# Kernel optimization log

Hardware: AMD Instinct MI355X
Metric: run time of the kernel (lower is better)

The kernel has to match this reference:

```python
import jax, jax.numpy as jnp
import numpy as np

B, S, D, H, DH = 2, 4096, 768, 12, 64
L = 2                      # encoder layers (reduced-depth longformer-base)
HW = 256                   # one-sided sliding window (attention_window = 512)
C = 2 * HW                 # query chunk size
NC = S // C                # number of chunks
KW = C + 2 * HW            # key-window length per chunk
V = 50265
SEP_ID, NSEP = 2, 32       # </s> token id; SEPs per block (fixed by construction)
G = NSEP + 1               # global tokens: <s> at pos 0 + all SEPs
NCLS = 5
EPS = 1e-5
NEG = -1e9


def layer_norm(x, gb):
    m = jnp.mean(x, -1, keepdims=True)
    v = jnp.var(x, -1, keepdims=True)
    return (x - m) * jax.lax.rsqrt(v + EPS) * gb[0] + gb[1]


def split_heads(x):  # [B,S,D] -> [B,H,S,DH]
    return x.reshape(B, S, H, DH).transpose(0, 2, 1, 3)


def window_gather(x):  # [B,H,S,DH] -> [B,H,NC,KW,DH] overlapping key windows
    xp = jnp.pad(x, ((0, 0), (0, 0), (HW, HW), (0, 0)))
    idx = (jnp.arange(NC) * C)[:, None] + jnp.arange(KW)[None, :]
    return xp[:, :, idx, :]


def longformer_attn(x, amask, gpos, wqkv, bqkv, wqkv_g, bqkv_g, wo, bo):
    q = split_heads(x @ wqkv[0] + bqkv[0]) / np.float32(np.sqrt(DH))
    k = split_heads(x @ wqkv[1] + bqkv[1])
    v = split_heads(x @ wqkv[2] + bqkv[2])

    # ----- local sliding-window scores (banded, chunked) -----
    kw = window_gather(k)
    vw = window_gather(v)
    qc = q.reshape(B, H, NC, C, DH)
    s_loc = jnp.einsum('bhncd,bhnkd->bhnck', qc, kw)  # [B,H,NC,C,KW]

    rel = jnp.arange(KW)[None, :] - jnp.arange(C)[:, None]          # [C,KW]
    band_ok = (rel >= 0) & (rel <= 2 * HW)
    key_pos = (jnp.arange(NC) * C)[:, None] + jnp.arange(KW)[None, :] - HW
    in_b = (key_pos >= 0) & (key_pos < S)                            # [NC,KW]
    amp = jnp.pad(amask, ((0, 0), (HW, HW)))
    idx = (jnp.arange(NC) * C)[:, None] + jnp.arange(KW)[None, :]
    am_w = amp[:, idx] > 0                                           # [B,NC,KW]
    mask = band_ok[None, None, None] & in_b[None, None, :, None, :] & am_w[:, None, :, None, :]
    s_loc = jnp.where(mask, s_loc, NEG).reshape(B, H, S, KW)

    # ----- scores of every query against the G global keys -----
    gidx = gpos[:, None, :, None]                                    # [B,1,G,1]
    kg = jnp.take_along_axis(k, gidx, axis=2)                        # [B,H,G,DH]
    vg = jnp.take_along_axis(v, gidx, axis=2)
    s_glob = jnp.einsum('bhsd,bhgd->bhsg', q, kg)                    # [B,H,S,G]

    probs = jax.nn.softmax(jnp.concatenate([s_glob, s_loc], -1), -1)
    pg, pl = probs[..., :G], probs[..., G:]
    ctx = jnp.einsum('bhsg,bhgd->bhsd', pg, vg)
    ctx = ctx + jnp.einsum('bhnck,bhnkd->bhncd', pl.reshape(B, H, NC, C, KW), vw).reshape(B, H, S, DH)

    # ----- global tokens attend to everything (separate projections) -----
    qg = split_heads(x @ wqkv_g[0] + bqkv_g[0]) / np.float32(np.sqrt(DH))
    kgf = split_heads(x @ wqkv_g[1] + bqkv_g[1])
    vgf = split_heads(x @ wqkv_g[2] + bqkv_g[2])
    qg = jnp.take_along_axis(qg, gidx, axis=2)                       # [B,H,G,DH]
    s_g = jnp.einsum('bhgd,bhsd->bhgs', qg, kgf)                     # [B,H,G,S]
    s_g = jnp.where(amask[:, None, None, :] > 0, s_g, NEG)
    og = jnp.einsum('bhgs,bhsd->bhgd', jax.nn.softmax(s_g, -1), vgf)

    ctx_m = ctx.transpose(0, 2, 1, 3).reshape(B, S, D)
    og_m = og.transpose(0, 2, 1, 3).reshape(B, G, D)
    ctx_m = ctx_m.at[jnp.arange(B)[:, None], gpos].set(og_m)         # replace global rows
    return ctx_m @ wo + bo


def setup_inputs() -> dict:
    key = jax.random.key(0)
    ks = jax.random.split(key, 12)
    ids = jax.random.randint(ks[0], (B, S), 5, V, dtype=jnp.int32)
    sep_positions = (jnp.arange(NSEP) + 1) * (S // NSEP) - 1         # SEP every 128 toks
    ids = ids.at[:, sep_positions].set(SEP_ID).at[:, 0].set(0)       # <s> at pos 0
    att = jnp.ones((B, S), jnp.int32)

    def nrm(k, shp):
        return jax.random.normal(k, shp, jnp.float32) * 0.02

    ln = jnp.stack([jnp.ones(D, jnp.float32), jnp.zeros(D, jnp.float32)])
    return dict(
        input_ids=ids, attention_mask=att,
        word_emb=nrm(ks[1], (V, D)), pos_emb=nrm(ks[2], (S + 2, D)),
        type_emb=nrm(ks[3], (D,)), emb_ln=ln,
        Wqkv=nrm(ks[4], (L, 3, D, D)), bqkv=jnp.zeros((L, 3, D), jnp.float32),
        Wqkv_g=nrm(ks[5], (L, 3, D, D)), bqkv_g=jnp.zeros((L, 3, D), jnp.float32),
        Wo=nrm(ks[6], (L, D, D)), bo=jnp.zeros((L, D), jnp.float32),
        ln1=jnp.broadcast_to(ln, (L, 2, D)),
        Wff1=nrm(ks[7], (L, D, 4 * D)), bff1=jnp.zeros((L, 4 * D), jnp.float32),
        Wff2=nrm(ks[8], (L, 4 * D, D)), bff2=jnp.zeros((L, D), jnp.float32),
        ln2=jnp.broadcast_to(ln, (L, 2, D)),
        cls_W=nrm(ks[9], (NCLS, D)), cls_b=jnp.zeros((NCLS,), jnp.float32),
    )


def reference(input_ids, attention_mask, word_emb, pos_emb, type_emb, emb_ln,
              Wqkv, bqkv, Wqkv_g, bqkv_g, Wo, bo, ln1, Wff1, bff1, Wff2, bff2,
              ln2, cls_W, cls_b):
    # global attention mask: pos 0 + every SEP (fixed count by construction)
    sep_pos = jnp.sort(jnp.where(input_ids == SEP_ID, jnp.arange(S)[None, :], S), -1)[:, :NSEP]
    sep_pos = sep_pos.astype(jnp.int32)
    gpos = jnp.concatenate([jnp.zeros((B, 1), jnp.int32), sep_pos], 1)  # [B,G]

    x = word_emb[input_ids] + pos_emb[jnp.arange(S) + 2][None] + type_emb
    x = layer_norm(x, emb_ln)
    for l in range(L):
        a = longformer_attn(x, attention_mask, gpos, Wqkv[l], bqkv[l],
                            Wqkv_g[l], bqkv_g[l], Wo[l], bo[l])
        x = layer_norm(x + a, ln1[l])
        f = jax.nn.gelu(x @ Wff1[l] + bff1[l], approximate=False) @ Wff2[l] + bff2[l]
        x = layer_norm(x + f, ln2[l])

    # gather SEP embeddings (row-major over batch then sentence) -> classifier
    h = jnp.take_along_axis(x, sep_pos[:, :, None], axis=1).reshape(B * NSEP, D)
    return h @ cls_W.T + cls_b
```

## Files before the change

### kernel.cpp

```cpp
#include <hip/hip_runtime.h>


#define Bb 2
#define Ss 4096
#define Dd 768
#define Hh 12
#define Gg 33
#define NSEPn 32
#define Ll 2
#define SPAD 4640
#define PADL 256
#define NCLSn 5
#define NCH 16
#define PARTF 1056
#define PSTR 72

typedef unsigned short u16;
typedef __attribute__((ext_vector_type(8))) short bv8;
typedef __attribute__((ext_vector_type(4))) short sv4;
typedef __attribute__((ext_vector_type(4))) float f32x4;

__device__ __forceinline__ float bf2f(u16 u) {
  unsigned v = ((unsigned)u) << 16;
  return __builtin_bit_cast(float, v);
}
__device__ __forceinline__ u16 f2bf(float f) {
  unsigned u = __builtin_bit_cast(unsigned, f);
  u += 0x7fffu + ((u >> 16) & 1u);
  return (u16)(u >> 16);
}
__device__ __forceinline__ void glds16(const void* g, void* l) {
  __builtin_amdgcn_global_load_lds(
      (const __attribute__((address_space(1))) void*)g,
      (__attribute__((address_space(3))) void*)l, 16, 0, 0);
}

__global__ void sep_find_kernel(const int* __restrict__ ids, int* __restrict__ cnt,
                                int* __restrict__ list) {
  int i = blockIdx.x * 256 + threadIdx.x;
  if (i >= Bb * Ss) return;
  int b = i >> 12;
  if (ids[i] == 2) {
    int idx = atomicAdd(&cnt[b], 1);
    if (idx < 64) list[b * 64 + idx] = i & (Ss - 1);
  }
}

__global__ void sep_sort_kernel(const int* __restrict__ cnt, const int* __restrict__ list,
                                int* __restrict__ gpos) {
  int b = blockIdx.x;
  int t = threadIdx.x;
  int n = cnt[b]; if (n > 64) n = 64;
  if (t < Gg) gpos[b * Gg + t] = (t == 0) ? 0 : (Ss - 1);
  __syncthreads();
  if (t < n) {
    int v = list[b * 64 + t];
    int rank = 0;
    for (int j = 0; j < n; ++j) rank += (list[b * 64 + j] < v) ? 1 : 0;
    if (rank < NSEPn) gpos[b * Gg + 1 + rank] = v;
  }
}

__global__ __launch_bounds__(256)
void wconv_kernel(const float* __restrict__ src0, u16* __restrict__ dst0,
                  int K, int N, int grp, int sstr, long unit, long WLs) {
  __shared__ float t[32][33];
  int z = blockIdx.z;
  const float* src = src0 + (size_t)((z / grp) * sstr + (z % grp)) * K * N;
  u16* dst = dst0 + (size_t)(z / grp) * WLs + (size_t)(z % grp) * unit;
  int n0 = blockIdx.x * 32, k0 = blockIdx.y * 32;
  int tx = threadIdx.x & 31, ty = threadIdx.x >> 5;
  #pragma unroll
  for (int i = 0; i < 4; ++i)
    t[ty + i * 8][tx] = src[(size_t)(k0 + ty + i * 8) * N + n0 + tx];
  __syncthreads();
  #pragma unroll
  for (int i = 0; i < 4; ++i)
    dst[(size_t)(n0 + ty + i * 8) * K + k0 + tx] = f2bf(t[tx][ty + i * 8]);
}

__global__ __launch_bounds__(256)
void embed_ln_kernel(const int* __restrict__ ids, const float* __restrict__ we,
                     const float* __restrict__ pe, const float* __restrict__ te,
                     const float* __restrict__ lnp, float* __restrict__ x,
                     u16* __restrict__ xb) {
  int row = blockIdx.x;
  int s = row & (Ss - 1);
  int id = ids[row];
  int tid = threadIdx.x;
  float v[3]; float sm = 0.f, s2 = 0.f;
  #pragma unroll
  for (int i = 0; i < 3; ++i) {
    int c = tid + i * 256;
    float t = we[(size_t)id * Dd + c] + pe[(size_t)(s + 2) * Dd + c] + te[c];
    v[i] = t; sm += t; s2 += t * t;
  }
  __shared__ float r1[256], r2[256];
  r1[tid] = sm; r2[tid] = s2; __syncthreads();
  for (int o = 128; o; o >>= 1) {
    if (tid < o) { r1[tid] += r1[tid + o]; r2[tid] += r2[tid + o]; }
    __syncthreads();
  }
  float mean = r1[0] * (1.f / 768.f);
  float var  = r2[0] * (1.f / 768.f) - mean * mean;
  float rs = rsqrtf(var + 1e-5f);
  #pragma unroll
  for (int i = 0; i < 3; ++i) {
    int c = tid + i * 256;
    float o = (v[i] - mean) * rs * lnp[c] + lnp[Dd + c];
    x[(size_t)row * Dd + c] = o;
    xb[(size_t)row * Dd + c] = f2bf(o);
  }
}

__global__ __launch_bounds__(256)
void add_ln3_kernel(const float* __restrict__ xin, const float* __restrict__ y0,
                    const float* __restrict__ y1, const float* __restrict__ lnp,
                    float* __restrict__ xout, u16* __restrict__ xbout) {
  int row = blockIdx.x;
  int tid = threadIdx.x;
  float v[3]; float sm = 0.f, s2 = 0.f;
  #pragma unroll
  for (int i = 0; i < 3; ++i) {
    int c = tid + i * 256;
    size_t idx = (size_t)row * Dd + c;
    float t = xin[idx] + y0[idx] + y1[idx];
    v[i] = t; sm += t; s2 += t * t;
  }
  __shared__ float r1[256], r2[256];
  r1[tid] = sm; r2[tid] = s2; __syncthreads();
  for (int o = 128; o; o >>= 1) {
    if (tid < o) { r1[tid] += r1[tid + o]; r2[tid] += r2[tid + o]; }
    __syncthreads();
  }
  float mean = r1[0] * (1.f / 768.f);
  float var  = r2[0] * (1.f / 768.f) - mean * mean;
  float rs = rsqrtf(var + 1e-5f);
  #pragma unroll
  for (int i = 0; i < 3; ++i) {
    int c = tid + i * 256;
    float o = (v[i] - mean) * rs * lnp[c] + lnp[Dd + c];
    xout[(size_t)row * Dd + c] = o;
    xbout[(size_t)row * Dd + c] = f2bf(o);
  }
}

template <int MODE, bool XSWZ>
__global__ __launch_bounds__(256)
void gemm2_kernel(const u16* __restrict__ A, const u16* __restrict__ Bt,
                  const float* __restrict__ bias, float* __restrict__ outf,
                  float* __restrict__ outf2,
                  u16* __restrict__ o0, u16* __restrict__ o1, u16* __restrict__ o2,
                  u16* __restrict__ o3, u16* __restrict__ o4,
                  int N, int Ks, int Kl, float scale) {
  __shared__ u16 la[2][128 * 32], lb[2][128 * 32];
  int tid = threadIdx.x;
  int wave = tid >> 6, lane = tid & 63;
  int wr = wave >> 1, wc = wave & 1;
  int lg = lane >> 4, lc = lane & 15;
  int bx = blockIdx.x, by = blockIdx.y;
  if (XSWZ) {
    int gx = gridDim.x;
    int nlin = bx + gx * by;
    int NB = gx * gridDim.y;
    nlin = (nlin & 7) * (NB >> 3) + (nlin >> 3);
    bx = nlin % gx;
    by = nlin / gx;
  }
  int row0 = by * 128, col0 = bx * 128;
  int koff = blockIdx.z * Kl;

  int sgr = (lane & 3) ^ ((lane >> 3) & 3);
  const u16* Ag = A + (size_t)(row0 + wave * 32 + (lane >> 2)) * Ks + sgr * 8 + koff;
  const u16* Bg = Bt + (size_t)(col0 + wave * 32 + (lane >> 2)) * Ks + sgr * 8 + koff;
  int wofs = wave * 1024;
  int gph = (lg ^ ((lc >> 1) & 3)) * 8;

  f32x4 acc[4][4];
  #pragma unroll
  for (int m = 0; m < 4; ++m)
    #pragma unroll
    for (int n = 0; n < 4; ++n) acc[m][n] = (f32x4){0.f, 0.f, 0.f, 0.f};

  glds16(Ag, la[0] + wofs);
  glds16(Ag + (size_t)16 * Ks, la[0] + wofs + 512);
  glds16(Bg, lb[0] + wofs);
  glds16(Bg + (size_t)16 * Ks, lb[0] + wofs + 512);
  __syncthreads();

  int nk = Kl >> 5;
  for (int t = 0; t < nk; ++t) {
    int cur = t & 1;
    if (t + 1 < nk) {
      int k1 = (t + 1) << 5;
      glds16(Ag + k1, la[cur ^ 1] + wofs);
      glds16(Ag + (size_t)16 * Ks + k1, la[cur ^ 1] + wofs + 512);
      glds16(Bg + k1, lb[cur ^ 1] + wofs);
      glds16(Bg + (size_t)16 * Ks + k1, lb[cur ^ 1] + wofs + 512);
    }
    bv8 af[4], bf_[4];
    #pragma unroll
    for (int m = 0; m < 4; ++m)
      af[m] = *reinterpret_cast<const bv8*>(la[cur] + (wr * 64 + m * 16 + lc) * 32 + gph);
    #pragma unroll
    for (int n = 0; n < 4; ++n)
      bf_[n] = *reinterpret_cast<const bv8*>(lb[cur] + (wc * 64 + n * 16 + lc) * 32 + gph);
    __builtin_amdgcn_s_setprio(1);
    #pragma unroll
    for (int m = 0; m < 4; ++m)
      #pragma unroll
      for (int n = 0; n < 4; ++n)
        acc[m][n] = __builtin_amdgcn_mfma_f32_16x16x32_bf16(af[m], bf_[n], acc[m][n], 0, 0, 0);
    __builtin_amdgcn_s_setprio(0);
    __syncthreads();
  }

  #pragma unroll
  for (int m = 0; m < 4; ++m) {
    int grow0 = row0 + wr * 64 + m * 16 + lg * 4;
    #pragma unroll
    for (int n = 0; n < 4; ++n) {
      int gcol = col0 + wc * 64 + n * 16 + lc;
      float bvl = bias[gcol];
      if (MODE == 0) {
        float* od = blockIdx.z ? outf2 : outf;
        float badd = blockIdx.z ? 0.f : bvl;
        #pragma unroll
        for (int r = 0; r < 4; ++r)
          od[(size_t)(grow0 + r) * N + gcol] = acc[m][n][r] + badd;
      } else if (MODE == 1) {
        #pragma unroll
        for (int r = 0; r < 4; ++r) {
          float v = acc[m][n][r] + bvl;
          v = 0.5f * v * (1.0f + erff(v * 0.70710678118654752f));
          o0[(size_t)(grow0 + r) * N + gcol] = f2bf(v);
        }
      } else if (MODE == 4) {
        #pragma unroll
        for (int r = 0; r < 4; ++r)
          o0[(size_t)(grow0 + r) * N + gcol] = f2bf((acc[m][n][r] + bvl) * scale);
      } else if (MODE == 2) {
        int sec = (col0 >> 7) / 6;
        int colr = gcol - sec * 768;
        int hh = colr >> 6, d = colr & 63;
        int bb = grow0 >> 12, s = grow0 & (Ss - 1);
        size_t bhh = (size_t)(bb * Hh + hh);
        if (sec == 0) {
          #pragma unroll
          for (int r = 0; r < 4; ++r)
            o0[(bhh * Ss + s + r) * 64 + d] = f2bf((acc[m][n][r] + bvl) * scale);
        } else if (sec == 1) {
          #pragma unroll
          for (int r = 0; r < 4; ++r)
            o1[(bhh * SPAD + PADL + s + r) * 64 + d] = f2bf(acc[m][n][r] + bvl);
        } else if (sec == 2) {
          sv4 pk;
          #pragma unroll
          for (int r = 0; r < 4; ++r) pk[r] = (short)f2bf(acc[m][n][r] + bvl);
          *reinterpret_cast<sv4*>(o2 + (bhh * 64 + d) * SPAD + PADL + s) = pk;
        } else if (sec == 3) {
          #pragma unroll
          for (int r = 0; r < 4; ++r)
            o3[(bhh * Ss + s + r) * 64 + d] = f2bf(acc[m][n][r] + bvl);
        } else {
          sv4 pk;
          #pragma unroll
          for (int r = 0; r < 4; ++r) pk[r] = (short)f2bf(acc[m][n][r] + bvl);
          *reinterpret_cast<sv4*>(o4 + (bhh * 64 + d) * Ss + s) = pk;
        }
      }
    }
  }
}

__global__ __launch_bounds__(256)
void gather_glob_kernel(const u16* __restrict__ kpk, const u16* __restrict__ vtpk,
                        const int* __restrict__ gpos, u16* __restrict__ kg,
                        u16* __restrict__ vgt) {
  int bh = blockIdx.x;
  int b = bh / Hh;
  int tid = threadIdx.x;
  for (int idx = tid; idx < 64 * 64; idx += 256) {
    int g = idx >> 6, d = idx & 63;
    u16 kv = 0, vv = 0;
    if (g < Gg) {
      int p = gpos[b * Gg + g];
      kv = kpk[((size_t)bh * SPAD + PADL + p) * 64 + d];
      vv = vtpk[((size_t)bh * 64 + d) * SPAD + PADL + p];
    }
    kg[(size_t)bh * 4096 + idx] = kv;
    vgt[((size_t)bh * 64 + d) * 64 + g] = vv;
  }
}

__global__ __launch_bounds__(256)
void gather_xg_kernel(const u16* __restrict__ xb, const int* __restrict__ gpos,
                      u16* __restrict__ xg) {
  int rg = blockIdx.x;
  int b = rg / Gg;
  int p = gpos[rg];
  int tid = threadIdx.x;
  for (int c = tid; c < Dd; c += 256)
    xg[(size_t)rg * Dd + c] = xb[((size_t)b * Ss + p) * Dd + c];
}

#define LOCAL_NB (Bb * Hh * (Ss / 64))
__global__ __launch_bounds__(256)
void attn_local_kernel(const u16* __restrict__ qpk, const u16* __restrict__ kpk,
                       const u16* __restrict__ vtpk, const u16* __restrict__ kg,
                       const u16* __restrict__ vgt, const int* __restrict__ amask,
                       u16* __restrict__ ctx) {
  __shared__ u16 Plds[4][16 * PSTR];
  int bid = blockIdx.x;
  int swz = (bid & 7) * (LOCAL_NB / 8) + (bid >> 3);
  int qb = swz & 63;
  int bh = swz >> 6;
  int b = bh / Hh;
  int h = bh - b * Hh;
  int wv = threadIdx.x >> 6;
  int q0 = qb * 64 + wv * 16;
  int lane = threadIdx.x & 63;
  int lg = lane >> 4, lc = lane & 15;
  int lg4 = lg * 4;
  int q = q0 + lc;

  const u16* qbase = qpk + (((size_t)bh) * Ss + q0) * 64;
  bv8 aq0 = *reinterpret_cast<const bv8*>(qbase + (size_t)lc * 64 + lg * 8);
  bv8 aq1 = *reinterpret_cast<const bv8*>(qbase + (size_t)lc * 64 + 32 + lg * 8);

  f32x4 o[4];
  #pragma unroll
  for (int i = 0; i < 4; ++i) o[i] = (f32x4){0.f, 0.f, 0.f, 0.f};
  float mrun = -1e30f, lrun = 0.f;

  const u16* kgb = kg + ((size_t)bh) * 64 * 64;
  const u16* vgb = vgt + ((size_t)bh) * 64 * 64;
  const u16* kb = kpk + ((size_t)bh) * SPAD * 64;
  const u16* vb = vtpk + ((size_t)bh) * 64 * SPAD;
  const int* amb = amask + b * Ss;
  u16* P = &Plds[wv][0];

  bv8 kc[8];
  #pragma unroll
  for (int j = 0; j < 4; ++j) {
    const u16* kr = kgb + (size_t)(j * 16 + lc) * 64;
    kc[2 * j]     = *reinterpret_cast<const bv8*>(kr + lg * 8);
    kc[2 * j + 1] = *reinterpret_cast<const bv8*>(kr + 32 + lg * 8);
  }
  int amvN;
  { int ni = min(max(q0 - 256 + lane, 0), Ss - 1); amvN = amb[ni]; }

  for (int step = 0; step < 10; ++step) {
    bool isg = (step == 0);
    int ks = isg ? 0 : (q0 - 256 + (step - 1) * 64);
    int amvC = amvN;
    if (step < 9) { int ni = min(max(q0 - 256 + step * 64 + lane, 0), Ss - 1); amvN = amb[ni]; }

    bv8 vf[8];
    #pragma unroll
    for (int j2 = 0; j2 < 2; ++j2)
      #pragma unroll
      for (int nt = 0; nt < 4; ++nt) {
        const u16* vr = isg ? (vgb + (size_t)(nt * 16 + lc) * 64 + j2 * 32)
                            : (vb + (size_t)(nt * 16 + lc) * SPAD + PADL + ks + j2 * 32);
        vf[j2 * 4 + nt] = *reinterpret_cast<const bv8*>(vr + lg * 8);
      }
    unsigned long long kmask;
    if (isg) {
      kmask = (1ull << Gg) - 1;
    } else {
      int kidx = ks + lane;
      kmask = __ballot((kidx >= 0) && (kidx < Ss) && (amvC > 0));
    }
    f32x4 sc[4];
    __builtin_amdgcn_s_setprio(1);
    #pragma unroll
    for (int j = 0; j < 4; ++j) {
      f32x4 z = (f32x4){0.f, 0.f, 0.f, 0.f};
      sc[j] = __builtin_amdgcn_mfma_f32_16x16x32_bf16(kc[2 * j], aq0, z, 0, 0, 0);
      sc[j] = __builtin_amdgcn_mfma_f32_16x16x32_bf16(kc[2 * j + 1], aq1, sc[j], 0, 0, 0);
    }
    __builtin_amdgcn_s_setprio(0);
    if (step < 9) {
      int ksn = q0 - 256 + step * 64;
      #pragma unroll
      for (int j = 0; j < 4; ++j) {
        const u16* kr = kb + (size_t)(PADL + ksn + j * 16 + lc) * 64;
        kc[2 * j]     = *reinterpret_cast<const bv8*>(kr + lg * 8);
        kc[2 * j + 1] = *reinterpret_cast<const bv8*>(kr + 32 + lg * 8);
      }
    }
    float mloc = -1e30f;
    bool fast = (!isg) && (step >= 2) && (step <= 8) && (kmask == ~0ull);
    if (fast) {
      #pragma unroll
      for (int j = 0; j < 4; ++j)
        #pragma unroll
        for (int r = 0; r < 4; ++r) mloc = fmaxf(mloc, sc[j][r]);
    } else {
      #pragma unroll
      for (int j = 0; j < 4; ++j)
        #pragma unroll
        for (int r = 0; r < 4; ++r) {
          int kk = ks + j * 16 + lg4 + r;
          bool ok = (kmask >> (j * 16 + lg4 + r)) & 1;
          if (!isg) ok = ok && ((unsigned)(kk - q + 256) <= 512u);
          sc[j][r] = ok ? sc[j][r] : -1e9f;
          mloc = fmaxf(mloc, sc[j][r]);
        }
    }
    mloc = fmaxf(mloc, __shfl_xor(mloc, 16));
    mloc = fmaxf(mloc, __shfl_xor(mloc, 32));
    if (__any(mloc > mrun)) {
      float nm = fmaxf(mrun, mloc);
      float scal = __expf(mrun - nm);
      mrun = nm;
      lrun *= scal;
      #pragma unroll
      for (int r = 0; r < 4; ++r) {
        float sr = __shfl(scal, lg4 + r);
        #pragma unroll
        for (int nt = 0; nt < 4; ++nt) o[nt][r] *= sr;
      }
    }
    float psum = 0.f;
    #pragma unroll
    for (int j = 0; j < 4; ++j) {
      sv4 pk;
      #pragma unroll
      for (int r = 0; r < 4; ++r) {
        float p = __expf(sc[j][r] - mrun);
        psum += p;
        pk[r] = (short)f2bf(p);
      }
      *reinterpret_cast<sv4*>(P + lc * PSTR + j * 16 + lg4) = pk;
    }
    psum += __shfl_xor(psum, 16);
    psum += __shfl_xor(psum, 32);
    lrun += psum;
    __builtin_amdgcn_s_setprio(1);
    #pragma unroll
    for (int j2 = 0; j2 < 2; ++j2) {
      bv8 ap = *reinterpret_cast<const bv8*>(P + lc * PSTR + j2 * 32 + lg * 8);
      #pragma unroll
      for (int nt = 0; nt < 4; ++nt)
        o[nt] = __builtin_amdgcn_mfma_f32_16x16x32_bf16(ap, vf[j2 * 4 + nt], o[nt], 0, 0, 0);
    }
    __builtin_amdgcn_s_setprio(0);
  }
  float inv = 1.0f / lrun;
  #pragma unroll
  for (int r = 0; r < 4; ++r) {
    float invr = __shfl(inv, lg4 + r);
    size_t rowoff = ((size_t)b * Ss + q0 + lg4 + r) * Dd + h * 64;
    #pragma unroll
    for (int nt = 0; nt < 4; ++nt)
      ctx[rowoff + nt * 16 + lc] = f2bf(o[nt][r] * invr);
  }
}

__global__ __launch_bounds__(192)
void attn_globalq_kernel(const u16* __restrict__ qgb, const u16* __restrict__ kgf,
                         const u16* __restrict__ vgt, const int* __restrict__ amask,
                         float* __restrict__ part) {
  __shared__ u16 Plds[3][16 * 32];
  int blk = blockIdx.x;
  int ch = blk & (NCH - 1);
  int bh = blk / NCH;
  int b = bh / Hh, h = bh - b * Hh;
  int wv = threadIdx.x >> 6;
  int lane = threadIdx.x & 63;
  int lg = lane >> 4, lc = lane & 15;

  int qrow = wv * 16 + lc;
  bv8 aq0 = (bv8)0, aq1 = (bv8)0;
  if (qrow < Gg) {
    const u16* qr = qgb + (size_t)(b * Gg + qrow) * Dd + h * 64;
    aq0 = *reinterpret_cast<const bv8*>(qr + lg * 8);
    aq1 = *reinterpret_cast<const bv8*>(qr + 32 + lg * 8);
  }

  f32x4 o[4];
  float mrun[4], lrun[4];
  #pragma unroll
  for (int i = 0; i < 4; ++i) { o[i] = (f32x4){0.f,0.f,0.f,0.f}; mrun[i] = -1e30f; lrun[i] = 0.f; }

  const u16* kb = kgf + ((size_t)bh) * Ss * 64;
  const u16* vb = vgt + ((size_t)bh) * 64 * Ss;
  const int* amb = amask + b * Ss;
  int ks0 = ch * (Ss / NCH);

  for (int st = 0; st < (Ss / NCH) / 32; ++st) {
    int ks = ks0 + st * 32;
    f32x4 sc0, sc1;
    {
      const u16* kr0 = kb + (size_t)(ks + lc) * 64;
      const u16* kr1 = kr0 + 16 * 64;
      bv8 b00 = *reinterpret_cast<const bv8*>(kr0 + lg * 8);
      bv8 b01 = *reinterpret_cast<const bv8*>(kr0 + 32 + lg * 8);
      bv8 b10 = *reinterpret_cast<const bv8*>(kr1 + lg * 8);
      bv8 b11 = *reinterpret_cast<const bv8*>(kr1 + 32 + lg * 8);
      f32x4 z = (f32x4){0.f,0.f,0.f,0.f};
      sc0 = __builtin_amdgcn_mfma_f32_16x16x32_bf16(aq0, b00, z, 0, 0, 0);
      sc0 = __builtin_amdgcn_mfma_f32_16x16x32_bf16(aq1, b01, sc0, 0, 0, 0);
      sc1 = __builtin_amdgcn_mfma_f32_16x16x32_bf16(aq0, b10, z, 0, 0, 0);
      sc1 = __builtin_amdgcn_mfma_f32_16x16x32_bf16(aq1, b11, sc1, 0, 0, 0);
    }
    bool v0 = amb[ks + lc] > 0;
    bool v1 = amb[ks + 16 + lc] > 0;
    #pragma unroll
    for (int r = 0; r < 4; ++r) {
      float s0 = v0 ? sc0[r] : -1e9f;
      float s1 = v1 ? sc1[r] : -1e9f;
      float rm = fmaxf(s0, s1);
      #pragma unroll
      for (int off = 1; off < 16; off <<= 1) rm = fmaxf(rm, __shfl_xor(rm, off));
      float nm = fmaxf(mrun[r], rm);
      float scal = __expf(mrun[r] - nm);
      float p0 = __expf(s0 - nm);
      float p1 = __expf(s1 - nm);
      float ps = p0 + p1;
      #pragma unroll
      for (int off = 1; off < 16; off <<= 1) ps += __shfl_xor(ps, off);
      lrun[r] = lrun[r] * scal + ps;
      mrun[r] = nm;
      #pragma unroll
      for (int nt = 0; nt < 4; ++nt) o[nt][r] *= scal;
      int prow = lg * 4 + r;
      Plds[wv][prow * 32 + lc] = f2bf(p0);
      Plds[wv][prow * 32 + 16 + lc] = f2bf(p1);
    }
    bv8 ap = *reinterpret_cast<const bv8*>(&Plds[wv][lc * 32 + lg * 8]);
    #pragma unroll
    for (int nt = 0; nt < 4; ++nt) {
      const u16* vr = vb + (size_t)(nt * 16 + lc) * Ss + ks;
      bv8 bvv = *reinterpret_cast<const bv8*>(vr + lg * 8);
      o[nt] = __builtin_amdgcn_mfma_f32_16x16x32_bf16(ap, bvv, o[nt], 0, 0, 0);
    }
  }

  float* pb = part + ((size_t)(bh * 3 + wv) * NCH + ch) * PARTF;
  #pragma unroll
  for (int r = 0; r < 4; ++r) {
    int row = lg * 4 + r;
    #pragma unroll
    for (int nt = 0; nt < 4; ++nt)
      pb[row * 64 + nt * 16 + lc] = o[nt][r];
    if (lc == 0) {
      pb[1024 + row] = mrun[r];
      pb[1040 + row] = lrun[r];
    }
  }
}

__global__ __launch_bounds__(256)
void attn_gmerge_kernel(const float* __restrict__ part, const int* __restrict__ gpos,
                        u16* __restrict__ ctx) {
  __shared__ float wgt[Gg][NCH];
  __shared__ float sinvl[Gg];
  int bh = blockIdx.x;
  int b = bh / Hh, h = bh - b * Hh;
  int tid = threadIdx.x;
  if (tid < Gg) {
    int qt = tid >> 4, rr = tid & 15;
    const float* pb = part + ((size_t)(bh * 3 + qt) * NCH) * PARTF;
    float mx = -1e30f;
    for (int c = 0; c < NCH; ++c) mx = fmaxf(mx, pb[c * PARTF + 1024 + rr]);
    float l = 0.f;
    for (int c = 0; c < NCH; ++c) {
      float w = __expf(pb[c * PARTF + 1024 + rr] - mx);
      wgt[tid][c] = w;
      l += w * pb[c * PARTF + 1040 + rr];
    }
    sinvl[tid] = 1.0f / l;
  }
  __syncthreads();
  for (int e = tid; e < Gg * 64; e += 256) {
    int row = e >> 6, d = e & 63;
    int qt = row >> 4, rr = row & 15;
    const float* pb = part + ((size_t)(bh * 3 + qt) * NCH) * PARTF + rr * 64 + d;
    float acc = 0.f;
    #pragma unroll
    for (int c = 0; c < NCH; ++c) acc += wgt[row][c] * pb[c * PARTF];
    int pos = gpos[b * Gg + row];
    ctx[((size_t)b * Ss + pos) * Dd + h * 64 + d] = f2bf(acc * sinvl[row]);
  }
}

__global__ __launch_bounds__(64)
void cls_kernel(const float* __restrict__ x, const float* __restrict__ W,
                const float* __restrict__ bias, const int* __restrict__ gpos,
                float* __restrict__ out) {
  int r = blockIdx.x;
  int b = r >> 5, i = r & 31;
  int pos = gpos[b * Gg + 1 + i];
  int lane = threadIdx.x;
  const float* xr = x + ((size_t)b * Ss + pos) * Dd;
  float acc[NCLSn] = {0.f, 0.f, 0.f, 0.f, 0.f};
  for (int k = lane; k < Dd; k += 64) {
    float xv = xr[k];
    #pragma unroll
    for (int c = 0; c < NCLSn; ++c) acc[c] += xv * W[c * Dd + k];
  }
  #pragma unroll
  for (int c = 0; c < NCLSn; ++c) {
    #pragma unroll
    for (int off = 1; off < 64; off <<= 1) acc[c] += __shfl_xor(acc[c], off);
  }
  if (lane == 0) {
    #pragma unroll
    for (int c = 0; c < NCLSn; ++c) out[r * NCLSn + c] = acc[c] + bias[c];
  }
}

extern "C" void kernel_launch(void* const* d_in, const int* in_sizes, int n_in,
                              void* d_out, int out_size, void* d_ws, size_t ws_size,
                              hipStream_t stream) {
  const int* ids     = (const int*)d_in[0];
  const int* amask   = (const int*)d_in[1];
  const float* we    = (const float*)d_in[2];
  const float* pe    = (const float*)d_in[3];
  const float* te    = (const float*)d_in[4];
  const float* embln = (const float*)d_in[5];
  const float* Wqkv  = (const float*)d_in[6];
  const float* bqkv  = (const float*)d_in[7];
  const float* Wqkvg = (const float*)d_in[8];
  const float* bqkvg = (const float*)d_in[9];
  const float* Wo    = (const float*)d_in[10];
  const float* bo    = (const float*)d_in[11];
  const float* ln1   = (const float*)d_in[12];
  const float* Wff1  = (const float*)d_in[13];
  const float* bff1  = (const float*)d_in[14];
  const float* Wff2  = (const float*)d_in[15];
  const float* bff2  = (const float*)d_in[16];
  const float* ln2   = (const float*)d_in[17];
  const float* clsW  = (const float*)d_in[18];
  const float* clsb  = (const float*)d_in[19];
  float* out = (float*)d_out;

  char* ws = (char*)d_ws;
  size_t off = 0;
  auto alloc = [&](size_t bytes) { size_t o = off; off += (bytes + 255) & ~(size_t)255; return o; };

  const size_t DD = (size_t)Dd * Dd;
  const size_t DF = (size_t)Dd * 4 * Dd;
  const size_t WL = 7 * DD + 2 * DF;

  size_t o_cnt  = alloc(Bb * 4);
  size_t o_list = alloc(Bb * 64 * 4);
  size_t o_gpos = alloc(Bb * Gg * 4);
  size_t o_bias = alloc((size_t)Ll * 3840 * 4);
  size_t o_w    = alloc(WL * Ll * 2);
  size_t o_x    = alloc((size_t)Bb * Ss * Dd * 4);
  size_t o_xb   = alloc((size_t)Bb * Ss * Dd * 2);
  size_t o_kgf  = alloc((size_t)Bb * Hh * Ss * 64 * 2);
  size_t o_vgf  = alloc((size_t)Bb * Hh * Ss * 64 * 2);
  size_t o_accB = o_kgf;
  size_t o_qpk  = alloc((size_t)Bb * Hh * Ss * 64 * 2);
  size_t o_kpk  = alloc((size_t)Bb * Hh * SPAD * 64 * 2);
  size_t o_vtpk = alloc((size_t)Bb * Hh * 64 * SPAD * 2);
  size_t o_kg   = alloc((size_t)Bb * Hh * 64 * 64 * 2);
  size_t o_vgt  = alloc((size_t)Bb * Hh * 64 * 64 * 2);
  size_t o_xg   = alloc((size_t)128 * Dd * 2);
  size_t o_qg   = alloc((size_t)128 * Dd * 2);
  size_t o_part = alloc((size_t)Bb * Hh * 3 * NCH * PARTF * 4);
  size_t o_f1b  = o_qpk;
  {
    size_t f1b_bytes = (size_t)Bb * Ss * 4 * Dd * 2;
    if (off - o_qpk < f1b_bytes) off = o_qpk + ((f1b_bytes + 255) & ~(size_t)255);
  }
  size_t o_ctx = alloc((size_t)Bb * Ss * Dd * 2);
  size_t o_acc = alloc((size_t)Bb * Ss * Dd * 4);
  if (ws_size < off) return;

  u16* Wb = (u16*)(ws + o_w);
  int* gposp = (int*)(ws + o_gpos);
  float* accA = (float*)(ws + o_acc);
  float* accB = (float*)(ws + o_accB);

  (void)hipMemsetAsync(ws + o_cnt, 0, Bb * 4, stream);
  (void)hipMemsetAsync(ws + o_kpk, 0, (size_t)Bb * Hh * SPAD * 64 * 2, stream);
  (void)hipMemsetAsync(ws + o_vtpk, 0, (size_t)Bb * Hh * 64 * SPAD * 2, stream);
  (void)hipMemsetAsync(ws + o_xg, 0, (size_t)128 * Dd * 2, stream);

  for (int l = 0; l < Ll; ++l) {
    (void)hipMemcpyAsync(ws + o_bias + (size_t)l * 3840 * 4, bqkv + (size_t)l * 3 * Dd,
                         3 * Dd * 4, hipMemcpyDeviceToDevice, stream);
    (void)hipMemcpyAsync(ws + o_bias + (size_t)l * 3840 * 4 + 3 * Dd * 4,
                         bqkvg + (size_t)(l * 3 + 1) * Dd,
                         2 * Dd * 4, hipMemcpyDeviceToDevice, stream);
  }

  sep_find_kernel<<<(Bb * Ss + 255) / 256, 256, 0, stream>>>(ids, (int*)(ws + o_cnt), (int*)(ws + o_list));
  sep_sort_kernel<<<Bb, 64, 0, stream>>>((int*)(ws + o_cnt), (int*)(ws + o_list), gposp);

  wconv_kernel<<<dim3(24, 24, 6), 256, 0, stream>>>(Wqkv,       Wb,          Dd, Dd, 3, 3, (long)DD, (long)WL);
  wconv_kernel<<<dim3(24, 24, 2), 256, 0, stream>>>(Wqkvg + DD,     Wb + 3 * DD, Dd, Dd, 1, 3, 0L, (long)WL);
  wconv_kernel<<<dim3(24, 24, 2), 256, 0, stream>>>(Wqkvg + 2 * DD, Wb + 4 * DD, Dd, Dd, 1, 3, 0L, (long)WL);
  wconv_kernel<<<dim3(24, 24, 2), 256, 0, stream>>>(Wqkvg,          Wb + 5 * DD, Dd, Dd, 1, 3, 0L, (long)WL);
  wconv_kernel<<<dim3(24, 24, 2), 256, 0, stream>>>(Wo,         Wb + 6 * DD, Dd, Dd, 1, 1, 0L, (long)WL);
  wconv_kernel<<<dim3(96, 24, 2), 256, 0, stream>>>(Wff1,       Wb + 7 * DD, Dd, 4 * Dd, 1, 1, 0L, (long)WL);
  wconv_kernel<<<dim3(24, 96, 2), 256, 0, stream>>>(Wff2,       Wb + 7 * DD + DF, 4 * Dd, Dd, 1, 1, 0L, (long)WL);

  embed_ln_kernel<<<Bb * Ss, 256, 0, stream>>>(ids, we, pe, te, embln, (float*)(ws + o_x), (u16*)(ws + o_xb));

  for (int l = 0; l < Ll; ++l) {
    size_t wb = (size_t)l * WL;
    u16* xb = (u16*)(ws + o_xb);
    gemm2_kernel<2, true><<<dim3(30, 64), 256, 0, stream>>>(xb, Wb + wb, (float*)(ws + o_bias) + (size_t)l * 3840,
        nullptr, nullptr,
        (u16*)(ws + o_qpk), (u16*)(ws + o_kpk), (u16*)(ws + o_vtpk),
        (u16*)(ws + o_kgf), (u16*)(ws + o_vgf), 3840, Dd, Dd, 0.125f);
    gather_glob_kernel<<<Bb * Hh, 256, 0, stream>>>((u16*)(ws + o_kpk), (u16*)(ws + o_vtpk), gposp, (u16*)(ws + o_kg), (u16*)(ws + o_vgt));
    gather_xg_kernel<<<Bb * Gg, 256, 0, stream>>>(xb, gposp, (u16*)(ws + o_xg));
    gemm2_kernel<4, false><<<dim3(6, 1), 256, 0, stream>>>((u16*)(ws + o_xg), Wb + wb + 5 * DD, bqkvg + (size_t)l * 3 * Dd,
        nullptr, nullptr, (u16*)(ws + o_qg), nullptr, nullptr, nullptr, nullptr, Dd, Dd, Dd, 0.125f);
    attn_local_kernel<<<LOCAL_NB, 256, 0, stream>>>((u16*)(ws + o_qpk), (u16*)(ws + o_kpk), (u16*)(ws + o_vtpk), (u16*)(ws + o_kg), (u16*)(ws + o_vgt), amask, (u16*)(ws + o_ctx));
    attn_globalq_kernel<<<Bb * Hh * NCH, 192, 0, stream>>>((u16*)(ws + o_qg), (u16*)(ws + o_kgf), (u16*)(ws + o_vgf), amask, (float*)(ws + o_part));
    attn_gmerge_kernel<<<Bb * Hh, 256, 0, stream>>>((float*)(ws + o_part), gposp, (u16*)(ws + o_ctx));
    gemm2_kernel<0, true><<<dim3(6, 64, 2), 256, 0, stream>>>((u16*)(ws + o_ctx), Wb + wb + 6 * DD, bo + (size_t)l * Dd, accA, accB,
        nullptr, nullptr, nullptr, nullptr, nullptr, Dd, Dd, Dd / 2, 1.0f);
    add_ln3_kernel<<<Bb * Ss, 256, 0, stream>>>((float*)(ws + o_x), accA, accB, ln1 + (size_t)l * 2 * Dd, (float*)(ws + o_x), xb);
    gemm2_kernel<1, true><<<dim3(24, 64), 256, 0, stream>>>(xb, Wb + wb + 7 * DD, bff1 + (size_t)l * 4 * Dd, nullptr, nullptr,
        (u16*)(ws + o_f1b), nullptr, nullptr, nullptr, nullptr, 4 * Dd, Dd, Dd, 1.0f);
    gemm2_kernel<0, true><<<dim3(6, 64, 2), 256, 0, stream>>>((u16*)(ws + o_f1b), Wb + wb + 7 * DD + DF, bff2 + (size_t)l * Dd, accA, accB,
        nullptr, nullptr, nullptr, nullptr, nullptr, Dd, 4 * Dd, 2 * Dd, 1.0f);
    add_ln3_kernel<<<Bb * Ss, 256, 0, stream>>>((float*)(ws + o_x), accA, accB, ln2 + (size_t)l * 2 * Dd, (float*)(ws + o_x), xb);
  }

  cls_kernel<<<Bb * NSEPn, 64, 0, stream>>>((float*)(ws + o_x), clsW, clsb, gposp, out);
}
```

Before: 852.6 us.

## Store second split-K partial as bf16 and restructure global-query attention loop

The second split-K partial of the output and FFN2 GEMMs is now written as bf16 instead of fp32, which halves that write and its later read in add_ln3 at some cost in precision. The global-query attention kernel is rewritten to process 64-key steps, prefetch K fragments a step ahead, use a ballot mask and a single shared running max per query row, and skip rescaling when the max does not change. The local attention kernel splits its V fragment loads so the second half is issued after the score MFMAs, which lowers register pressure.

```diff
diff --git a/kernel.cpp b/kernel.cpp
--- a/kernel.cpp
+++ b/kernel.cpp
@@ -115,7 +115,7 @@
 
 __global__ __launch_bounds__(256)
 void add_ln3_kernel(const float* __restrict__ xin, const float* __restrict__ y0,
-                    const float* __restrict__ y1, const float* __restrict__ lnp,
+                    const u16* __restrict__ y1, const float* __restrict__ lnp,
                     float* __restrict__ xout, u16* __restrict__ xbout) {
   int row = blockIdx.x;
   int tid = threadIdx.x;
@@ -124,7 +124,7 @@
   for (int i = 0; i < 3; ++i) {
     int c = tid + i * 256;
     size_t idx = (size_t)row * Dd + c;
-    float t = xin[idx] + y0[idx] + y1[idx];
+    float t = xin[idx] + y0[idx] + bf2f(y1[idx]);
     v[i] = t; sm += t; s2 += t * t;
   }
   __shared__ float r1[256], r2[256];
@@ -149,7 +149,6 @@
 __global__ __launch_bounds__(256)
 void gemm2_kernel(const u16* __restrict__ A, const u16* __restrict__ Bt,
                   const float* __restrict__ bias, float* __restrict__ outf,
-                  float* __restrict__ outf2,
                   u16* __restrict__ o0, u16* __restrict__ o1, u16* __restrict__ o2,
                   u16* __restrict__ o3, u16* __restrict__ o4,
                   int N, int Ks, int Kl, float scale) {
@@ -223,11 +222,15 @@
       int gcol = col0 + wc * 64 + n * 16 + lc;
       float bvl = bias[gcol];
       if (MODE == 0) {
-        float* od = blockIdx.z ? outf2 : outf;
-        float badd = blockIdx.z ? 0.f : bvl;
-        #pragma unroll
-        for (int r = 0; r < 4; ++r)
-          od[(size_t)(grow0 + r) * N + gcol] = acc[m][n][r] + badd;
+        if (blockIdx.z == 0) {
+          #pragma unroll
+          for (int r = 0; r < 4; ++r)
+            outf[(size_t)(grow0 + r) * N + gcol] = acc[m][n][r] + bvl;
+        } else {
+          #pragma unroll
+          for (int r = 0; r < 4; ++r)
+            o0[(size_t)(grow0 + r) * N + gcol] = f2bf(acc[m][n][r]);
+        }
       } else if (MODE == 1) {
         #pragma unroll
         for (int r = 0; r < 4; ++r) {
@@ -356,15 +359,13 @@
     int amvC = amvN;
     if (step < 9) { int ni = min(max(q0 - 256 + step * 64 + lane, 0), Ss - 1); amvN = amb[ni]; }
 
-    bv8 vf[8];
-    #pragma unroll
-    for (int j2 = 0; j2 < 2; ++j2)
-      #pragma unroll
-      for (int nt = 0; nt < 4; ++nt) {
-        const u16* vr = isg ? (vgb + (size_t)(nt * 16 + lc) * 64 + j2 * 32)
-                            : (vb + (size_t)(nt * 16 + lc) * SPAD + PADL + ks + j2 * 32);
-        vf[j2 * 4 + nt] = *reinterpret_cast<const bv8*>(vr + lg * 8);
-      }
+    bv8 vf0[4];
+    #pragma unroll
+    for (int nt = 0; nt < 4; ++nt) {
+      const u16* vr = isg ? (vgb + (size_t)(nt * 16 + lc) * 64)
+                          : (vb + (size_t)(nt * 16 + lc) * SPAD + PADL + ks);
+      vf0[nt] = *reinterpret_cast<const bv8*>(vr + lg * 8);
+    }
     unsigned long long kmask;
     if (isg) {
       kmask = (1ull << Gg) - 1;
@@ -381,6 +382,13 @@
       sc[j] = __builtin_amdgcn_mfma_f32_16x16x32_bf16(kc[2 * j + 1], aq1, sc[j], 0, 0, 0);
     }
     __builtin_amdgcn_s_setprio(0);
+    bv8 vf1[4];
+    #pragma unroll
+    for (int nt = 0; nt < 4; ++nt) {
+      const u16* vr = isg ? (vgb + (size_t)(nt * 16 + lc) * 64 + 32)
+                          : (vb + (size_t)(nt * 16 + lc) * SPAD + PADL + ks + 32);
+      vf1[nt] = *reinterpret_cast<const bv8*>(vr + lg * 8);
+    }
     if (step < 9) {
       int ksn = q0 - 256 + step * 64;
       #pragma unroll
@@ -439,12 +447,15 @@
     psum += __shfl_xor(psum, 32);
     lrun += psum;
     __builtin_amdgcn_s_setprio(1);
-    #pragma unroll
-    for (int j2 = 0; j2 < 2; ++j2) {
-      bv8 ap = *reinterpret_cast<const bv8*>(P + lc * PSTR + j2 * 32 + lg * 8);
+    {
+      bv8 ap = *reinterpret_cast<const bv8*>(P + lc * PSTR + lg * 8);
       #pragma unroll
       for (int nt = 0; nt < 4; ++nt)
-        o[nt] = __builtin_amdgcn_mfma_f32_16x16x32_bf16(ap, vf[j2 * 4 + nt], o[nt], 0, 0, 0);
+        o[nt] = __builtin_amdgcn_mfma_f32_16x16x32_bf16(ap, vf0[nt], o[nt], 0, 0, 0);
+      ap = *reinterpret_cast<const bv8*>(P + lc * PSTR + 32 + lg * 8);
+      #pragma unroll
+      for (int nt = 0; nt < 4; ++nt)
+        o[nt] = __builtin_amdgcn_mfma_f32_16x16x32_bf16(ap, vf1[nt], o[nt], 0, 0, 0);
     }
     __builtin_amdgcn_s_setprio(0);
   }
@@ -463,7 +474,7 @@
 void attn_globalq_kernel(const u16* __restrict__ qgb, const u16* __restrict__ kgf,
                          const u16* __restrict__ vgt, const int* __restrict__ amask,
                          float* __restrict__ part) {
-  __shared__ u16 Plds[3][16 * 32];
+  __shared__ u16 Plds[3][16 * PSTR];
   int blk = blockIdx.x;
   int ch = blk & (NCH - 1);
   int bh = blk / NCH;
@@ -471,6 +482,7 @@
   int wv = threadIdx.x >> 6;
   int lane = threadIdx.x & 63;
   int lg = lane >> 4, lc = lane & 15;
+  int lg4 = lg * 4;
 
   int qrow = wv * 16 + lc;
   bv8 aq0 = (bv8)0, aq1 = (bv8)0;
@@ -481,75 +493,122 @@
   }
 
   f32x4 o[4];
-  float mrun[4], lrun[4];
-  #pragma unroll
-  for (int i = 0; i < 4; ++i) { o[i] = (f32x4){0.f,0.f,0.f,0.f}; mrun[i] = -1e30f; lrun[i] = 0.f; }
+  #pragma unroll
+  for (int i = 0; i < 4; ++i) o[i] = (f32x4){0.f, 0.f, 0.f, 0.f};
+  float mrun = -1e30f, lrun = 0.f;
 
   const u16* kb = kgf + ((size_t)bh) * Ss * 64;
   const u16* vb = vgt + ((size_t)bh) * 64 * Ss;
   const int* amb = amask + b * Ss;
   int ks0 = ch * (Ss / NCH);
-
-  for (int st = 0; st < (Ss / NCH) / 32; ++st) {
-    int ks = ks0 + st * 32;
-    f32x4 sc0, sc1;
-    {
-      const u16* kr0 = kb + (size_t)(ks + lc) * 64;
-      const u16* kr1 = kr0 + 16 * 64;
-      bv8 b00 = *reinterpret_cast<const bv8*>(kr0 + lg * 8);
-      bv8 b01 = *reinterpret_cast<const bv8*>(kr0 + 32 + lg * 8);
-      bv8 b10 = *reinterpret_cast<const bv8*>(kr1 + lg * 8);
-      bv8 b11 = *reinterpret_cast<const bv8*>(kr1 + 32 + lg * 8);
-      f32x4 z = (f32x4){0.f,0.f,0.f,0.f};
-      sc0 = __builtin_amdgcn_mfma_f32_16x16x32_bf16(aq0, b00, z, 0, 0, 0);
-      sc0 = __builtin_amdgcn_mfma_f32_16x16x32_bf16(aq1, b01, sc0, 0, 0, 0);
-      sc1 = __builtin_amdgcn_mfma_f32_16x16x32_bf16(aq0, b10, z, 0, 0, 0);
-      sc1 = __builtin_amdgcn_mfma_f32_16x16x32_bf16(aq1, b11, sc1, 0, 0, 0);
-    }
-    bool v0 = amb[ks + lc] > 0;
-    bool v1 = amb[ks + 16 + lc] > 0;
-    #pragma unroll
-    for (int r = 0; r < 4; ++r) {
-      float s0 = v0 ? sc0[r] : -1e9f;
-      float s1 = v1 ? sc1[r] : -1e9f;
-      float rm = fmaxf(s0, s1);
-      #pragma unroll
-      for (int off = 1; off < 16; off <<= 1) rm = fmaxf(rm, __shfl_xor(rm, off));
-      float nm = fmaxf(mrun[r], rm);
-      float scal = __expf(mrun[r] - nm);
-      float p0 = __expf(s0 - nm);
-      float p1 = __expf(s1 - nm);
-      float ps = p0 + p1;
-      #pragma unroll
-      for (int off = 1; off < 16; off <<= 1) ps += __shfl_xor(ps, off);
-      lrun[r] = lrun[r] * scal + ps;
-      mrun[r] = nm;
-      #pragma unroll
-      for (int nt = 0; nt < 4; ++nt) o[nt][r] *= scal;
-      int prow = lg * 4 + r;
-      Plds[wv][prow * 32 + lc] = f2bf(p0);
-      Plds[wv][prow * 32 + 16 + lc] = f2bf(p1);
-    }
-    bv8 ap = *reinterpret_cast<const bv8*>(&Plds[wv][lc * 32 + lg * 8]);
+  u16* P = &Plds[wv][0];
+
+  bv8 kc[8];
+  #pragma unroll
+  for (int j = 0; j < 4; ++j) {
+    const u16* kr = kb + (size_t)(ks0 + j * 16 + lc) * 64;
+    kc[2 * j]     = *reinterpret_cast<const bv8*>(kr + lg * 8);
+    kc[2 * j + 1] = *reinterpret_cast<const bv8*>(kr + 32 + lg * 8);
+  }
+
+  for (int st = 0; st < 4; ++st) {
+    int ks = ks0 + st * 64;
+    bv8 vf0[4], vf1[4];
     #pragma unroll
     for (int nt = 0; nt < 4; ++nt) {
       const u16* vr = vb + (size_t)(nt * 16 + lc) * Ss + ks;
-      bv8 bvv = *reinterpret_cast<const bv8*>(vr + lg * 8);
-      o[nt] = __builtin_amdgcn_mfma_f32_16x16x32_bf16(ap, bvv, o[nt], 0, 0, 0);
-    }
+      vf0[nt] = *reinterpret_cast<const bv8*>(vr + lg * 8);
+      vf1[nt] = *reinterpret_cast<const bv8*>(vr + 32 + lg * 8);
+    }
+    unsigned long long kmask = __ballot(amb[ks + lane] > 0);
+    f32x4 sc[4];
+    __builtin_amdgcn_s_setprio(1);
+    #pragma unroll
+    for (int j = 0; j < 4; ++j) {
+      f32x4 z = (f32x4){0.f, 0.f, 0.f, 0.f};
+      sc[j] = __builtin_amdgcn_mfma_f32_16x16x32_bf16(kc[2 * j], aq0, z, 0, 0, 0);
+      sc[j] = __builtin_amdgcn_mfma_f32_16x16x32_bf16(kc[2 * j + 1], aq1, sc[j], 0, 0, 0);
+    }
+    __builtin_amdgcn_s_setprio(0);
+    if (st < 3) {
+      int ksn = ks0 + (st + 1) * 64;
+      #pragma unroll
+      for (int j = 0; j < 4; ++j) {
+        const u16* kr = kb + (size_t)(ksn + j * 16 + lc) * 64;
+        kc[2 * j]     = *reinterpret_cast<const bv8*>(kr + lg * 8);
+        kc[2 * j + 1] = *reinterpret_cast<const bv8*>(kr + 32 + lg * 8);
+      }
+    }
+    float mloc = -1e30f;
+    if (kmask == ~0ull) {
+      #pragma unroll
+      for (int j = 0; j < 4; ++j)
+        #pragma unroll
+        for (int r = 0; r < 4; ++r) mloc = fmaxf(mloc, sc[j][r]);
+    } else {
+      #pragma unroll
+      for (int j = 0; j < 4; ++j)
+        #pragma unroll
+        for (int r = 0; r < 4; ++r) {
+          bool ok = (kmask >> (j * 16 + lg4 + r)) & 1;
+          sc[j][r] = ok ? sc[j][r] : -1e9f;
+          mloc = fmaxf(mloc, sc[j][r]);
+        }
+    }
+    mloc = fmaxf(mloc, __shfl_xor(mloc, 16));
+    mloc = fmaxf(mloc, __shfl_xor(mloc, 32));
+    if (__any(mloc > mrun)) {
+      float nm = fmaxf(mrun, mloc);
+      float scal = __expf(mrun - nm);
+      mrun = nm;
+      lrun *= scal;
+      #pragma unroll
+      for (int r = 0; r < 4; ++r) {
+        float sr = __shfl(scal, lg4 + r);
+        #pragma unroll
+        for (int nt = 0; nt < 4; ++nt) o[nt][r] *= sr;
+      }
+    }
+    float psum = 0.f;
+    #pragma unroll
+    for (int j = 0; j < 4; ++j) {
+      sv4 pk;
+      #pragma unroll
+      for (int r = 0; r < 4; ++r) {
+        float p = __expf(sc[j][r] - mrun);
+        psum += p;
+        pk[r] = (short)f2bf(p);
+      }
+      *reinterpret_cast<sv4*>(P + lc * PSTR + j * 16 + lg4) = pk;
+    }
+    psum += __shfl_xor(psum, 16);
+    psum += __shfl_xor(psum, 32);
+    lrun += psum;
+    __builtin_amdgcn_s_setprio(1);
+    {
+      bv8 ap = *reinterpret_cast<const bv8*>(P + lc * PSTR + lg * 8);
+      #pragma unroll
+      for (int nt = 0; nt < 4; ++nt)
+        o[nt] = __builtin_amdgcn_mfma_f32_16x16x32_bf16(ap, vf0[nt], o[nt], 0, 0, 0);
+      ap = *reinterpret_cast<const bv8*>(P + lc * PSTR + 32 + lg * 8);
+      #pragma unroll
+      for (int nt = 0; nt < 4; ++nt)
+        o[nt] = __builtin_amdgcn_mfma_f32_16x16x32_bf16(ap, vf1[nt], o[nt], 0, 0, 0);
+    }
+    __builtin_amdgcn_s_setprio(0);
   }
 
   float* pb = part + ((size_t)(bh * 3 + wv) * NCH + ch) * PARTF;
   #pragma unroll
   for (int r = 0; r < 4; ++r) {
-    int row = lg * 4 + r;
+    int row = lg4 + r;
     #pragma unroll
     for (int nt = 0; nt < 4; ++nt)
       pb[row * 64 + nt * 16 + lc] = o[nt][r];
-    if (lc == 0) {
-      pb[1024 + row] = mrun[r];
-      pb[1040 + row] = lrun[r];
-    }
+  }
+  if (lg == 0) {
+    pb[1024 + lc] = mrun;
+    pb[1040 + lc] = lrun;
   }
 }
 
@@ -676,7 +735,7 @@
   u16* Wb = (u16*)(ws + o_w);
   int* gposp = (int*)(ws + o_gpos);
   float* accA = (float*)(ws + o_acc);
-  float* accB = (float*)(ws + o_accB);
+  u16* accB = (u16*)(ws + o_accB);
 
   (void)hipMemsetAsync(ws + o_cnt, 0, Bb * 4, stream);
   (void)hipMemsetAsync(ws + o_kpk, 0, (size_t)Bb * Hh * SPAD * 64 * 2, stream);
@@ -708,23 +767,23 @@
     size_t wb = (size_t)l * WL;
     u16* xb = (u16*)(ws + o_xb);
     gemm2_kernel<2, true><<<dim3(30, 64), 256, 0, stream>>>(xb, Wb + wb, (float*)(ws + o_bias) + (size_t)l * 3840,
-        nullptr, nullptr,
+        nullptr,
         (u16*)(ws + o_qpk), (u16*)(ws + o_kpk), (u16*)(ws + o_vtpk),
         (u16*)(ws + o_kgf), (u16*)(ws + o_vgf), 3840, Dd, Dd, 0.125f);
     gather_glob_kernel<<<Bb * Hh, 256, 0, stream>>>((u16*)(ws + o_kpk), (u16*)(ws + o_vtpk), gposp, (u16*)(ws + o_kg), (u16*)(ws + o_vgt));
     gather_xg_kernel<<<Bb * Gg, 256, 0, stream>>>(xb, gposp, (u16*)(ws + o_xg));
     gemm2_kernel<4, false><<<dim3(6, 1), 256, 0, stream>>>((u16*)(ws + o_xg), Wb + wb + 5 * DD, bqkvg + (size_t)l * 3 * Dd,
-        nullptr, nullptr, (u16*)(ws + o_qg), nullptr, nullptr, nullptr, nullptr, Dd, Dd, Dd, 0.125f);
+        nullptr, (u16*)(ws + o_qg), nullptr, nullptr, nullptr, nullptr, Dd, Dd, Dd, 0.125f);
     attn_local_kernel<<<LOCAL_NB, 256, 0, stream>>>((u16*)(ws + o_qpk), (u16*)(ws + o_kpk), (u16*)(ws + o_vtpk), (u16*)(ws + o_kg), (u16*)(ws + o_vgt), amask, (u16*)(ws + o_ctx));
     attn_globalq_kernel<<<Bb * Hh * NCH, 192, 0, stream>>>((u16*)(ws + o_qg), (u16*)(ws + o_kgf), (u16*)(ws + o_vgf), amask, (float*)(ws + o_part));
     attn_gmerge_kernel<<<Bb * Hh, 256, 0, stream>>>((float*)(ws + o_part), gposp, (u16*)(ws + o_ctx));
-    gemm2_kernel<0, true><<<dim3(6, 64, 2), 256, 0, stream>>>((u16*)(ws + o_ctx), Wb + wb + 6 * DD, bo + (size_t)l * Dd, accA, accB,
-        nullptr, nullptr, nullptr, nullptr, nullptr, Dd, Dd, Dd / 2, 1.0f);
+    gemm2_kernel<0, true><<<dim3(6, 64, 2), 256, 0, stream>>>((u16*)(ws + o_ctx), Wb + wb + 6 * DD, bo + (size_t)l * Dd, accA,
+        accB, nullptr, nullptr, nullptr, nullptr, Dd, Dd, Dd / 2, 1.0f);
     add_ln3_kernel<<<Bb * Ss, 256, 0, stream>>>((float*)(ws + o_x), accA, accB, ln1 + (size_t)l * 2 * Dd, (float*)(ws + o_x), xb);
-    gemm2_kernel<1, true><<<dim3(24, 64), 256, 0, stream>>>(xb, Wb + wb + 7 * DD, bff1 + (size_t)l * 4 * Dd, nullptr, nullptr,
+    gemm2_kernel<1, true><<<dim3(24, 64), 256, 0, stream>>>(xb, Wb + wb + 7 * DD, bff1 + (size_t)l * 4 * Dd, nullptr,
         (u16*)(ws + o_f1b), nullptr, nullptr, nullptr, nullptr, 4 * Dd, Dd, Dd, 1.0f);
-    gemm2_kernel<0, true><<<dim3(6, 64, 2), 256, 0, stream>>>((u16*)(ws + o_f1b), Wb + wb + 7 * DD + DF, bff2 + (size_t)l * Dd, accA, accB,
-        nullptr, nullptr, nullptr, nullptr, nullptr, Dd, 4 * Dd, 2 * Dd, 1.0f);
+    gemm2_kernel<0, true><<<dim3(6, 64, 2), 256, 0, stream>>>((u16*)(ws + o_f1b), Wb + wb + 7 * DD + DF, bff2 + (size_t)l * Dd, accA,
+        accB, nullptr, nullptr, nullptr, nullptr, Dd, 4 * Dd, 2 * Dd, 1.0f);
     add_ln3_kernel<<<Bb * Ss, 256, 0, stream>>>((float*)(ws + o_x), accA, accB, ln2 + (size_t)l * 2 * Dd, (float*)(ws + o_x), xb);
   }
 
```

Result: no change. 840.4 us (-1.4%).
